# Optimization experiments

Measured on AMD Instinct MI355X. Metric: run time of the kernel, lower is better.

Reference implementation:

```python
import jax, jax.numpy as jnp
import numpy as np

# Config constants (MLAConfig)
B, S = 1, 2048                 # batch, context_len (prefill: seq == context_len)
H = 16                         # num_heads
DN, DR, DV = 128, 64, 128      # qk_nope_head_dim, qk_rope_head_dim, v_head_dim
QL, C = 1536, 512              # q_lora_rank, kv_lora_rank
BLK = 128                      # fp8 dequant block size
MAX_CACHE = 4096
SOFTMAX_SCALE = 1.0 / np.sqrt(DN + DR)  # 1/sqrt(192)
NEG_INF = -10000.0


def gen_rope(n_total, head_size):
    # theta_j = 10000^{-2j/d}; idx_theta[i, 0, :] = [i*theta, i*theta] (repeated halves)
    theta = 1.0 / (10000.0 ** (jnp.arange(0, head_size, 2, dtype=jnp.float32) / head_size))
    idx = jnp.outer(jnp.arange(n_total, dtype=jnp.float32), theta)  # (N, d/2)
    return jnp.tile(idx[:, None, :], (1, 1, 2))                     # (N, 1, d)


def fp8_dequant(x, s, block=BLK):
    # Block-wise dequant: x (M,N) * per-(block x block) scale s (M/b, N/b).
    M, N = x.shape
    m, n = M // block, N // block  # shapes chosen divisible by block -> no padding
    return (x.reshape(m, block, n, block) * s[:, None, :, None]).reshape(M, N)


def apply_rope(x, cos, sin):
    # x: (B*S, heads, d). Interleaved RoPE: de-interleave pairs into halves,
    # then x*cos + rotate_half(x)*sin with cos/sin (B*S, 1, d).
    bs, h, d = x.shape
    x = x.reshape(bs, h, d // 2, 2).transpose(0, 1, 3, 2).reshape(bs, h, d)
    rot = jnp.concatenate([-x[..., d // 2:], x[..., :d // 2]], axis=-1)
    return x * cos + rot * sin


def setup_inputs() -> dict:
    key = jax.random.key(0)
    ks = jax.random.split(key, 9)
    WUQ = jax.random.normal(ks[0], (H * (DN + DR), QL), dtype=jnp.float32)
    WUKV = jax.random.normal(ks[1], (H * (DN + DV), C), dtype=jnp.float32)
    # positive, small block scales so attention logits stay well-conditioned
    WUQ_scale = 0.05 * jax.random.uniform(ks[2], (H * (DN + DR) // BLK, QL // BLK), dtype=jnp.float32)
    WUKV_scale = 0.05 * jax.random.uniform(ks[3], (H * (DN + DV) // BLK, C // BLK), dtype=jnp.float32)
    Q = jax.random.normal(ks[4], (B, S, QL), dtype=jnp.float32)
    KV = jax.random.normal(ks[5], (B, S, C), dtype=jnp.float32)
    PE = jax.random.normal(ks[6], (B, S, DR), dtype=jnp.float32)
    kv_cache = jax.random.normal(ks[7], (B, MAX_CACHE, C), dtype=jnp.float32)
    pe_cache = jax.random.normal(ks[8], (B, MAX_CACHE, DR), dtype=jnp.float32)
    idx_theta = gen_rope(B * S, DR)
    mask = jnp.triu(jnp.full((S, S), NEG_INF, dtype=jnp.float32), k=1)
    return {"WUQ": WUQ, "WUQ_scale": WUQ_scale, "WUKV": WUKV, "WUKV_scale": WUKV_scale,
            "Q": Q, "KV": KV, "PE": PE, "kv_cache": kv_cache, "pe_cache": pe_cache,
            "idx_theta": idx_theta, "mask": mask}


def reference(WUQ, WUQ_scale, WUKV, WUKV_scale, Q, KV, PE, kv_cache, pe_cache, idx_theta, mask):
    bsz, seqlen, _ = Q.shape
    # fp8 block-wise dequant of the low-rank up-projection weights
    WUQd = fp8_dequant(WUQ, WUQ_scale)
    WUKVd = fp8_dequant(WUKV, WUKV_scale)
    # Q up-projection from q_lora latent: (B*S, QL) @ (QL, H*(DN+DR))
    q = (Q.reshape(-1, QL) @ WUQd.T).reshape(bsz, seqlen, H, DN + DR)
    q_nope, q_pe = q[..., :DN], q[..., DN:]
    cos, sin = jnp.cos(idx_theta), jnp.sin(idx_theta)  # (B*S, 1, DR)
    q_pe = apply_rope(q_pe.reshape(bsz * seqlen, H, DR), cos, sin).reshape(bsz, seqlen, H, DR)
    k_pe = apply_rope(PE.reshape(bsz * seqlen, 1, DR), cos, sin).reshape(bsz, seqlen, DR)
    # absorbed low-rank K matrix: q_nope projected into the kv latent space
    W3 = WUKVd.reshape(H, DN + DV, C)
    q_lat = jnp.einsum('bshd,hdc->bshc', q_nope, W3[:, :DN])
    # continuous-cache prefill: write fresh latents into the cache, attend over them
    kv = kv_cache.at[:, :seqlen].set(KV)[:, :seqlen]   # (B, S, C)
    pe = pe_cache.at[:, :seqlen].set(k_pe)[:, :seqlen]  # (B, S, DR)
    scores = (jnp.einsum('bshc,btc->bsht', q_lat, kv)
              + jnp.einsum('bshr,btr->bsht', q_pe, pe)) * SOFTMAX_SCALE
    scores = scores + mask[None, :, None, :]
    attn = jax.nn.softmax(scores, axis=-1)
    x = jnp.einsum('bsht,btc->bshc', attn, kv)
    out = jnp.einsum('bshc,hdc->bshd', x, W3[:, DN:])  # V up-projection (absorbed)
    return out  # (B, S, H, DV)
```

## Files before the change

### kernel.cpp

```cpp
#include <hip/hip_runtime.h>

typedef __bf16 bf16_t;
typedef __attribute__((ext_vector_type(4))) __bf16 bf16x4;
typedef __attribute__((ext_vector_type(8))) __bf16 bf16x8;
typedef __attribute__((ext_vector_type(4))) float f32x4;

#define SOFTMAX_SCALE 0.07216878364870322f
#define NEG_MASK (-10000.0f)

__device__ __forceinline__ void async16(const bf16_t* g, bf16_t* l) {
  __builtin_amdgcn_global_load_lds(
      (const __attribute__((address_space(1))) unsigned int*)g,
      (__attribute__((address_space(3))) unsigned int*)l, 16, 0, 0);
}

__global__ void k_prep(const float* __restrict__ WUQ, const float* __restrict__ WUQs,
                       bf16_t* __restrict__ WUQd,
                       const float* __restrict__ WUKV, const float* __restrict__ WUKVs,
                       bf16_t* __restrict__ WUKVd, bf16_t* __restrict__ Wv1t,
                       const float* __restrict__ Q, bf16_t* __restrict__ Qb,
                       const float* __restrict__ KV, bf16_t* __restrict__ K4,
                       bf16_t* __restrict__ V4,
                       const float* __restrict__ PE, const float* __restrict__ idxt) {
  __shared__ bf16_t Lt[64][72];
  const int b = blockIdx.x;
  const int tid = threadIdx.x;

  if (b < 4608) {
    int i = (b * 256 + tid) * 4;
    int r = i / 1536, c = i % 1536;
    float s = WUQs[(r >> 7) * 12 + (c >> 7)];
    float4 w = *(const float4*)(WUQ + i);
    WUQd[i + 0] = (bf16_t)(w.x * s);
    WUQd[i + 1] = (bf16_t)(w.y * s);
    WUQd[i + 2] = (bf16_t)(w.z * s);
    WUQd[i + 3] = (bf16_t)(w.w * s);
  } else if (b < 5632) {
    int i4 = ((b - 4608) * 256 + tid) * 4;
    int h = i4 >> 16, within = i4 & 65535;
    int row = 128 + (within >> 9), col = within & 511;
    int R = h * 256 + row;
    float s = WUKVs[(R >> 7) * 4 + (col >> 7)];
    const float* src = WUKV + (size_t)R * 512 + col;
    float4 w = *(const float4*)src;
    bf16_t* dst = WUKVd + (size_t)R * 512 + col;
    dst[0] = (bf16_t)(w.x * s);
    dst[1] = (bf16_t)(w.y * s);
    dst[2] = (bf16_t)(w.z * s);
    dst[3] = (bf16_t)(w.w * s);
  } else if (b < 8704) {
    int i = ((b - 5632) * 256 + tid) * 4;
    float4 v = *(const float4*)(Q + i);
    Qb[i + 0] = (bf16_t)(v.x * SOFTMAX_SCALE);
    Qb[i + 1] = (bf16_t)(v.y * SOFTMAX_SCALE);
    Qb[i + 2] = (bf16_t)(v.z * SOFTMAX_SCALE);
    Qb[i + 3] = (bf16_t)(v.w * SOFTMAX_SCALE);
  } else if (b < 8832) {
    int i = (b - 8704) * 256 + tid;
    int c2 = i & 15, t = i >> 4;
    int tt = t >> 6, k = t & 63;
    const float* src = KV + (size_t)t * 512 + c2 * 32;
    bf16_t* dst = K4 + (size_t)tt * 36864 + c2 * 2048 + k * 8;
#pragma unroll
    for (int sub = 0; sub < 4; ++sub) {
      float4 u = *(const float4*)(src + sub * 8);
      float4 v = *(const float4*)(src + sub * 8 + 4);
      bf16x8 o;
      o[0] = (bf16_t)u.x; o[1] = (bf16_t)u.y; o[2] = (bf16_t)u.z; o[3] = (bf16_t)u.w;
      o[4] = (bf16_t)v.x; o[5] = (bf16_t)v.y; o[6] = (bf16_t)v.z; o[7] = (bf16_t)v.w;
      *(bf16x8*)(dst + sub * 512) = o;
    }
  } else if (b < 9344) {
    int i = (b - 8832) * 256 + tid;
    int c = i & 511, a = i >> 9;
    int t0 = a * 8, tt = t0 >> 6;
    int key0 = t0 & 63, kk2 = key0 >> 5, sub = (key0 >> 3) & 3;
    bf16x8 o;
#pragma unroll
    for (int j = 0; j < 8; ++j)
      o[j] = (bf16_t)KV[(size_t)(t0 + j) * 512 + c];
    *(bf16x8*)(V4 + (size_t)tt * 32768 + kk2 * 16384 + sub * 4096 + c * 8) = o;
  } else if (b < 9600) {
    int i = (b - 9344) * 256 + tid;
    int t = i >> 5, j = i & 31;
    float a = idxt[t * 64 + j];
    float c1 = cosf(a), s1 = sinf(a);
    float e = PE[t * 64 + 2 * j], o = PE[t * 64 + 2 * j + 1];
    int tt = t >> 6, k = t & 63;
    bf16_t* base = K4 + (size_t)tt * 36864 + (j >> 3) * 512 + k * 8 + (j & 7);
    base[16 * 2048] = (bf16_t)(e * c1 - o * s1);
    base[17 * 2048] = (bf16_t)(o * c1 + e * s1);
  } else {
    int bb = b - 9600;
    int h = bb >> 4;
    int d0 = ((bb >> 3) & 1) * 64;
    int c0 = (bb & 7) * 64;
    float s = WUKVs[8 * h + (c0 >> 7)];
#pragma unroll
    for (int j = 0; j < 2; ++j) {
      int ch = tid * 2 + j, r = ch >> 3, c8 = ch & 7;
      const float* src = WUKV + (size_t)(h * 256 + d0 + r) * 512 + c0 + c8 * 8;
      float4 u = *(const float4*)src;
      float4 v = *(const float4*)(src + 4);
      bf16x8 o;
      o[0] = (bf16_t)(u.x * s); o[1] = (bf16_t)(u.y * s);
      o[2] = (bf16_t)(u.z * s); o[3] = (bf16_t)(u.w * s);
      o[4] = (bf16_t)(v.x * s); o[5] = (bf16_t)(v.y * s);
      o[6] = (bf16_t)(v.z * s); o[7] = (bf16_t)(v.w * s);
      *(bf16x8*)&Lt[r][c8 * 8] = o;
    }
    __syncthreads();
#pragma unroll
    for (int j = 0; j < 2; ++j) {
      int ch = tid * 2 + j, cc = ch >> 3, dd8 = ch & 7;
      bf16x8 o;
#pragma unroll
      for (int e = 0; e < 8; ++e) o[e] = Lt[dd8 * 8 + e][cc];
      *(bf16x8*)(Wv1t + (size_t)h * 65536 + (c0 + cc) * 128 + d0 + dd8 * 8) = o;
    }
  }
}

__global__ void k_q_rope(const bf16_t* __restrict__ q, const float* __restrict__ idxt,
                         bf16_t* __restrict__ qfull) {
  int i = blockIdx.x * 256 + threadIdx.x;
  int j = i & 31, h = (i >> 5) & 15, t = i >> 9;
  float a = idxt[t * 64 + j];
  float c1 = cosf(a), s1 = sinf(a);
  const bf16_t* src = q + t * 3072 + h * 192 + 128;
  float e = (float)src[2 * j], o = (float)src[2 * j + 1];
  bf16_t* dst = qfull + (size_t)h * 2048 * 576 + t * 576 + 512;
  dst[j]      = (bf16_t)(e * c1 - o * s1);
  dst[32 + j] = (bf16_t)(o * c1 + e * s1);
}

template <int OUT_F32>
__global__ __launch_bounds__(256) void k_gemm3(
    const bf16_t* __restrict__ A, int lda, long saz,
    const bf16_t* __restrict__ B, int ldb, long sbz,
    void* __restrict__ Cv, int ldc, long scz, int K) {
  __shared__ __attribute__((aligned(16))) bf16_t At[2][8192];
  __shared__ __attribute__((aligned(16))) bf16_t Bt[2][8192];
  const int tid = threadIdx.x;
  const int lane = tid & 63;
  const int wv = tid >> 6;
  const int fr = lane & 15, fq = lane >> 4;
  const int wm = (wv & 1) * 64, wn = (wv >> 1) * 64;
  const int m0 = blockIdx.x * 128, n0 = blockIdx.y * 128;
  const bf16_t* Ab = A + (long)blockIdx.z * saz;
  const bf16_t* Bb = B + (long)blockIdx.z * sbz;

#define STAGE3(bufp, ks)                                                    \
  do {                                                                      \
    _Pragma("unroll") for (int i_ = 0; i_ < 4; ++i_) {                      \
      int ch_ = tid + i_ * 256;                                             \
      int ar_ = ch_ >> 3;                                                   \
      int c8_ = (ch_ & 7) ^ (ar_ & 7);                                      \
      async16(Ab + (size_t)(m0 + ar_) * lda + (ks) * 64 + c8_ * 8,          \
              At[bufp] + ch_ * 8);                                          \
      async16(Bb + (size_t)(n0 + ar_) * ldb + (ks) * 64 + c8_ * 8,          \
              Bt[bufp] + ch_ * 8);                                          \
    }                                                                       \
  } while (0)

  f32x4 acc[4][4] = {};
  const int nks = K >> 6;
  STAGE3(0, 0);
  for (int ks = 0; ks < nks; ++ks) {
    int buf = ks & 1;
    __syncthreads();
    if (ks + 1 < nks) STAGE3(buf ^ 1, ks + 1);
#pragma unroll
    for (int kkl = 0; kkl < 2; ++kkl) {
      bf16x8 af[4], bfr[4];
#pragma unroll
      for (int m = 0; m < 4; ++m) {
        int row = wm + m * 16 + fr;
        af[m] = *(const bf16x8*)(At[buf] + (row * 8 + (((kkl * 4 + fq) ^ (row & 7)))) * 8);
      }
#pragma unroll
      for (int n = 0; n < 4; ++n) {
        int row = wn + n * 16 + fr;
        bfr[n] = *(const bf16x8*)(Bt[buf] + (row * 8 + (((kkl * 4 + fq) ^ (row & 7)))) * 8);
      }
#pragma unroll
      for (int m = 0; m < 4; ++m)
#pragma unroll
        for (int n = 0; n < 4; ++n)
          acc[m][n] = __builtin_amdgcn_mfma_f32_16x16x32_bf16(af[m], bfr[n], acc[m][n], 0, 0, 0);
    }
  }
#undef STAGE3
#pragma unroll
  for (int m = 0; m < 4; ++m) {
    int row = m0 + wm + m * 16 + fq * 4;
#pragma unroll
    for (int n = 0; n < 4; ++n) {
      int col = n0 + wn + n * 16 + fr;
#pragma unroll
      for (int i = 0; i < 4; ++i) {
        if (OUT_F32)
          ((float*)Cv)[(long)blockIdx.z * scz + (size_t)(row + i) * ldc + col] = acc[m][n][i];
        else
          ((bf16_t*)Cv)[(long)blockIdx.z * scz + (size_t)(row + i) * ldc + col] = (bf16_t)acc[m][n][i];
      }
    }
  }
}

__global__ __attribute__((amdgpu_flat_work_group_size(512, 512),
                          amdgpu_waves_per_eu(2, 2)))
void k_attn(const bf16_t* __restrict__ qfull,
            const bf16_t* __restrict__ K4,
            const bf16_t* __restrict__ V4,
            bf16_t* __restrict__ X) {
  __shared__ __attribute__((aligned(16))) bf16_t Kt[18 * 2048];
  __shared__ __attribute__((aligned(16))) bf16_t Vt[2 * 16384];
  __shared__ __attribute__((aligned(16))) bf16_t P[64 * 64];
  __shared__ __attribute__((aligned(16))) bf16_t Qpe[8 * 512];
  __shared__ float lred[4][64];

  const int tid = threadIdx.x;
  const int lane = tid & 63;
  const int w = tid >> 6;
  const int fr = lane & 15, fq = lane >> 4;
  const int h = blockIdx.x & 15;
  const int qt = 31 - (blockIdx.x >> 4);
  const int nt = qt + 1;
  const int rg = w >> 2;
  const int kq = w & 3;

  const bf16_t* qh = qfull + (size_t)h * 2048 * 576;
  bf16_t* Xh = X + (size_t)h * 2048 * 512;

  {
    int row = tid >> 3, sub = tid & 7;
    bf16x8 v = *(const bf16x8*)(qh + (size_t)(qt * 64 + row) * 576 + 512 + sub * 8);
    *(bf16x8*)(Qpe + sub * 512 + row * 8) = v;
  }

  bf16x8 qa[2][16];
  {
    const bf16_t* qb = qh + (size_t)(qt * 64 + rg * 32) * 576;
#pragma unroll
    for (int mf = 0; mf < 2; ++mf)
#pragma unroll
      for (int kk = 0; kk < 16; ++kk)
        qa[mf][kk] = *(const bf16x8*)(qb + (mf * 16 + fr) * 576 + kk * 32 + fq * 8);
  }

#pragma unroll
  for (int i = 0; i < 9; ++i) {
    int ck = w + 8 * i;
    async16(K4 + ck * 512 + lane * 8, Kt + ck * 512 + lane * 8);
  }

  f32x4 acc[2][8] = {};
  float lreg[2] = {0.f, 0.f};

  for (int t = 0; t < nt; ++t) {
    __syncthreads();

    {
      const bf16_t* vsrc = V4 + (size_t)t * 32768;
#pragma unroll
      for (int i = 0; i < 8; ++i) {
        int cv = w + 8 * i;
        async16(vsrc + cv * 512 + lane * 8, Vt + cv * 512 + lane * 8);
      }
    }

    f32x4 sA[2] = {}, sB[2] = {};
    __builtin_amdgcn_s_setprio(1);
#pragma unroll
    for (int kk = 0; kk < 16; kk += 2) {
      bf16x8 kf0 = *(const bf16x8*)(Kt + kk * 2048 + fq * 512 + (kq * 16 + fr) * 8);
      bf16x8 kf1 = *(const bf16x8*)(Kt + (kk + 1) * 2048 + fq * 512 + (kq * 16 + fr) * 8);
      sA[0] = __builtin_amdgcn_mfma_f32_16x16x32_bf16(kf0, qa[0][kk], sA[0], 0, 0, 0);
      sA[1] = __builtin_amdgcn_mfma_f32_16x16x32_bf16(kf0, qa[1][kk], sA[1], 0, 0, 0);
      sB[0] = __builtin_amdgcn_mfma_f32_16x16x32_bf16(kf1, qa[0][kk + 1], sB[0], 0, 0, 0);
      sB[1] = __builtin_amdgcn_mfma_f32_16x16x32_bf16(kf1, qa[1][kk + 1], sB[1], 0, 0, 0);
    }
    {
      bf16x8 kf0 = *(const bf16x8*)(Kt + 16 * 2048 + fq * 512 + (kq * 16 + fr) * 8);
      bf16x8 kf1 = *(const bf16x8*)(Kt + 17 * 2048 + fq * 512 + (kq * 16 + fr) * 8);
      bf16x8 q00 = *(const bf16x8*)(Qpe + fq * 512 + (rg * 32 + fr) * 8);
      bf16x8 q01 = *(const bf16x8*)(Qpe + fq * 512 + (rg * 32 + 16 + fr) * 8);
      bf16x8 q10 = *(const bf16x8*)(Qpe + (4 + fq) * 512 + (rg * 32 + fr) * 8);
      bf16x8 q11 = *(const bf16x8*)(Qpe + (4 + fq) * 512 + (rg * 32 + 16 + fr) * 8);
      sA[0] = __builtin_amdgcn_mfma_f32_16x16x32_bf16(kf0, q00, sA[0], 0, 0, 0);
      sA[1] = __builtin_amdgcn_mfma_f32_16x16x32_bf16(kf0, q01, sA[1], 0, 0, 0);
      sB[0] = __builtin_amdgcn_mfma_f32_16x16x32_bf16(kf1, q10, sB[0], 0, 0, 0);
      sB[1] = __builtin_amdgcn_mfma_f32_16x16x32_bf16(kf1, q11, sB[1], 0, 0, 0);
    }
    __builtin_amdgcn_s_setprio(0);
    f32x4 s[2];
#pragma unroll
    for (int mf = 0; mf < 2; ++mf)
#pragma unroll
      for (int i = 0; i < 4; ++i) s[mf][i] = sA[mf][i] + sB[mf][i];

    bool diag = (t == qt);
#pragma unroll
    for (int mf = 0; mf < 2; ++mf) {
      int qrow = rg * 32 + mf * 16 + fr;
      if (diag) {
#pragma unroll
        for (int i = 0; i < 4; ++i) {
          int kcol = kq * 16 + fq * 4 + i;
          if (kcol > qrow) s[mf][i] += NEG_MASK;
        }
      }
      float p0 = __expf(s[mf][0]);
      float p1 = __expf(s[mf][1]);
      float p2 = __expf(s[mf][2]);
      float p3 = __expf(s[mf][3]);
      bf16x4 pk;
      pk[0] = (bf16_t)p0; pk[1] = (bf16_t)p1; pk[2] = (bf16_t)p2; pk[3] = (bf16_t)p3;
      int chunk = (kq * 2 + (fq >> 1)) ^ (qrow & 7);
      *(bf16x4*)(P + qrow * 64 + chunk * 8 + (fq & 1) * 4) = pk;
      lreg[mf] += (p0 + p1) + (p2 + p3);
    }
    __syncthreads();

    if (t + 1 < nt) {
      const bf16_t* ksrc = K4 + (size_t)(t + 1) * 36864;
#pragma unroll
      for (int i = 0; i < 9; ++i) {
        int ck = w + 8 * i;
        async16(ksrc + ck * 512 + lane * 8, Kt + ck * 512 + lane * 8);
      }
    }

    __builtin_amdgcn_s_setprio(1);
#pragma unroll
    for (int kk2 = 0; kk2 < 2; ++kk2) {
      bf16x8 pa[2];
#pragma unroll
      for (int mf = 0; mf < 2; ++mf) {
        int qrow = rg * 32 + mf * 16 + fr;
        pa[mf] = *(const bf16x8*)(P + qrow * 64 + (((kk2 * 4 + fq) ^ (qrow & 7)) * 8));
      }
#pragma unroll
      for (int nf = 0; nf < 8; ++nf) {
        bf16x8 vb = *(const bf16x8*)(Vt + kk2 * 16384 + fq * 4096 + (kq * 128 + nf * 16 + fr) * 8);
        acc[0][nf] = __builtin_amdgcn_mfma_f32_16x16x32_bf16(pa[0], vb, acc[0][nf], 0, 0, 0);
        acc[1][nf] = __builtin_amdgcn_mfma_f32_16x16x32_bf16(pa[1], vb, acc[1][nf], 0, 0, 0);
      }
    }
    __builtin_amdgcn_s_setprio(0);
  }

#pragma unroll
  for (int mf = 0; mf < 2; ++mf) {
    float lw = lreg[mf];
    lw += __shfl_xor(lw, 16);
    lw += __shfl_xor(lw, 32);
    if (fq == 0) lred[kq][rg * 32 + mf * 16 + fr] = lw;
  }
  __syncthreads();

  {
    bf16_t* XT = Kt;
#pragma unroll
    for (int mf = 0; mf < 2; ++mf)
#pragma unroll
      for (int i = 0; i < 4; ++i) {
        int row = rg * 32 + mf * 16 + fq * 4 + i;
        float invl = 1.0f / ((lred[0][row] + lred[1][row]) + (lred[2][row] + lred[3][row]));
#pragma unroll
        for (int nf = 0; nf < 8; ++nf)
          XT[row * 512 + kq * 128 + nf * 16 + fr] = (bf16_t)(acc[mf][nf][i] * invl);
      }
  }
  __syncthreads();
#pragma unroll
  for (int it = 0; it < 8; ++it) {
    int id = tid + it * 512;
    int row = id >> 6, j = id & 63;
    *(bf16x8*)(Xh + (size_t)(qt * 64 + row) * 512 + j * 8) = *(const bf16x8*)(Kt + row * 512 + j * 8);
  }
}


extern "C" void kernel_launch(void* const* d_in, const int* in_sizes, int n_in,
                              void* d_out, int out_size, void* d_ws, size_t ws_size,
                              hipStream_t stream) {
  (void)in_sizes; (void)n_in; (void)out_size; (void)ws_size;
  const float* WUQ   = (const float*)d_in[0];
  const float* WUQs  = (const float*)d_in[1];
  const float* WUKV  = (const float*)d_in[2];
  const float* WUKVs = (const float*)d_in[3];
  const float* Q     = (const float*)d_in[4];
  const float* KV    = (const float*)d_in[5];
  const float* PE    = (const float*)d_in[6];
  const float* idxt  = (const float*)d_in[9];
  float* out = (float*)d_out;

  char* ws = (char*)d_ws;
  size_t off = 0;
  auto alloc = [&](size_t n) -> char* {
    char* p = ws + off;
    off += (n + 255) & ~(size_t)255;
    return p;
  };
  bf16_t* WUQd  = (bf16_t*)alloc((size_t)3072 * 1536 * 2);
  bf16_t* Qb    = (bf16_t*)alloc((size_t)2048 * 1536 * 2);
  bf16_t* WUKVd = (bf16_t*)alloc((size_t)4096 * 512 * 2);
  bf16_t* Wv1t  = (bf16_t*)alloc((size_t)16 * 512 * 128 * 2);
  bf16_t* qbuf  = (bf16_t*)alloc((size_t)2048 * 3072 * 2);
  bf16_t* K4    = (bf16_t*)alloc((size_t)32 * 36864 * 2);
  bf16_t* V4    = (bf16_t*)alloc((size_t)32 * 32768 * 2);
  bf16_t* qfull = (bf16_t*)alloc((size_t)16 * 2048 * 576 * 2);
  bf16_t* Xb    = (bf16_t*)alloc((size_t)16 * 2048 * 512 * 2);

  k_prep<<<9856, 256, 0, stream>>>(WUQ, WUQs, WUQd, WUKV, WUKVs, WUKVd, Wv1t,
                                   Q, Qb, KV, K4, V4, PE, idxt);
  k_gemm3<0><<<dim3(16, 24, 1), 256, 0, stream>>>(Qb, 1536, 0, WUQd, 1536, 0,
                                                  qbuf, 3072, 0, 1536);
  k_q_rope<<<4096, 256, 0, stream>>>(qbuf, idxt, qfull);
  k_gemm3<0><<<dim3(16, 4, 16), 256, 0, stream>>>(qbuf, 3072, 192, Wv1t, 128, (long)512 * 128,
                                                  qfull, 576, (long)2048 * 576, 128);
  k_attn<<<dim3(512), dim3(512), 0, stream>>>(qfull, K4, V4, Xb);
  k_gemm3<1><<<dim3(16, 1, 16), 256, 0, stream>>>(Xb, 512, (long)2048 * 512,
                                                  WUKVd + 128 * 512, 512, (long)256 * 512,
                                                  out, 2048, 128, 512);
}
```

Baseline: 194.6 us.

## Software-pipeline attention loop: overlap next tile's QK with current softmax and PV

Restructures the causal attention tile loop into prologue/steady-state/epilogue so that QK^T MFMAs for tile t are interleaved with the exp/P-store of tile t-1 and followed by PV of tile t-1. The diagonal masking moves to the epilogue since only the last tile is diagonal. This aims to hide the softmax VALU latency behind matrix work. In exchange it keeps two score sets live, which raises register pressure, and it drops the split sA/sB accumulators that gave two independent MFMA chains. When nt==1 it issues a redundant K reload.

```diff
diff --git a/kernel.cpp b/kernel.cpp
--- a/kernel.cpp
+++ b/kernel.cpp
@@ -257,64 +257,127 @@
 
   f32x4 acc[2][8] = {};
   float lreg[2] = {0.f, 0.f};
-
-  for (int t = 0; t < nt; ++t) {
-    __syncthreads();
-
-    {
-      const bf16_t* vsrc = V4 + (size_t)t * 32768;
-#pragma unroll
-      for (int i = 0; i < 8; ++i) {
-        int cv = w + 8 * i;
-        async16(vsrc + cv * 512 + lane * 8, Vt + cv * 512 + lane * 8);
-      }
-    }
-
-    f32x4 sA[2] = {}, sB[2] = {};
+  f32x4 sO[2];
+
+#define QK_CHUNKS(K0, K1)                                                      \
+  do {                                                                         \
+    _Pragma("unroll") for (int kk = (K0); kk < (K1); ++kk) {                   \
+      bf16x8 kf = *(const bf16x8*)(Kt + kk * 2048 + fq * 512 + (kq * 16 + fr) * 8); \
+      sN[0] = __builtin_amdgcn_mfma_f32_16x16x32_bf16(kf, qa[0][kk], sN[0], 0, 0, 0); \
+      sN[1] = __builtin_amdgcn_mfma_f32_16x16x32_bf16(kf, qa[1][kk], sN[1], 0, 0, 0); \
+    }                                                                          \
+  } while (0)
+
+#define QK_PE()                                                                \
+  do {                                                                         \
+    _Pragma("unroll") for (int kk = 16; kk < 18; ++kk) {                       \
+      bf16x8 kf = *(const bf16x8*)(Kt + kk * 2048 + fq * 512 + (kq * 16 + fr) * 8); \
+      bf16x8 q0 = *(const bf16x8*)(Qpe + ((kk - 16) * 4 + fq) * 512 + (rg * 32 + fr) * 8); \
+      bf16x8 q1 = *(const bf16x8*)(Qpe + ((kk - 16) * 4 + fq) * 512 + (rg * 32 + 16 + fr) * 8); \
+      sN[0] = __builtin_amdgcn_mfma_f32_16x16x32_bf16(kf, q0, sN[0], 0, 0, 0);  \
+      sN[1] = __builtin_amdgcn_mfma_f32_16x16x32_bf16(kf, q1, sN[1], 0, 0, 0);  \
+    }                                                                          \
+  } while (0)
+
+#define EXP_P()                                                                \
+  do {                                                                         \
+    _Pragma("unroll") for (int mf = 0; mf < 2; ++mf) {                         \
+      int qrow = rg * 32 + mf * 16 + fr;                                       \
+      float p0 = __expf(sO[mf][0]);                                            \
+      float p1 = __expf(sO[mf][1]);                                            \
+      float p2 = __expf(sO[mf][2]);                                            \
+      float p3 = __expf(sO[mf][3]);                                            \
+      bf16x4 pk;                                                               \
+      pk[0] = (bf16_t)p0; pk[1] = (bf16_t)p1; pk[2] = (bf16_t)p2; pk[3] = (bf16_t)p3; \
+      int chunk = (kq * 2 + (fq >> 1)) ^ (qrow & 7);                           \
+      *(bf16x4*)(P + qrow * 64 + chunk * 8 + (fq & 1) * 4) = pk;               \
+      lreg[mf] += (p0 + p1) + (p2 + p3);                                       \
+    }                                                                          \
+  } while (0)
+
+#define PV()                                                                   \
+  do {                                                                         \
+    __builtin_amdgcn_s_setprio(1);                                             \
+    _Pragma("unroll") for (int kk2 = 0; kk2 < 2; ++kk2) {                      \
+      bf16x8 pa[2];                                                            \
+      _Pragma("unroll") for (int mf = 0; mf < 2; ++mf) {                       \
+        int qrow = rg * 32 + mf * 16 + fr;                                     \
+        pa[mf] = *(const bf16x8*)(P + qrow * 64 + (((kk2 * 4 + fq) ^ (qrow & 7)) * 8)); \
+      }                                                                        \
+      _Pragma("unroll") for (int nf = 0; nf < 8; ++nf) {                       \
+        bf16x8 vb = *(const bf16x8*)(Vt + kk2 * 16384 + fq * 4096 + (kq * 128 + nf * 16 + fr) * 8); \
+        acc[0][nf] = __builtin_amdgcn_mfma_f32_16x16x32_bf16(pa[0], vb, acc[0][nf], 0, 0, 0); \
+        acc[1][nf] = __builtin_amdgcn_mfma_f32_16x16x32_bf16(pa[1], vb, acc[1][nf], 0, 0, 0); \
+      }                                                                        \
+    }                                                                          \
+    __builtin_amdgcn_s_setprio(0);                                             \
+  } while (0)
+
+#define ISSUE_V(tv)                                                            \
+  do {                                                                         \
+    const bf16_t* vsrc_ = V4 + (size_t)(tv) * 32768;                           \
+    _Pragma("unroll") for (int i_ = 0; i_ < 8; ++i_) {                         \
+      int cv_ = w + 8 * i_;                                                    \
+      async16(vsrc_ + cv_ * 512 + lane * 8, Vt + cv_ * 512 + lane * 8);        \
+    }                                                                          \
+  } while (0)
+
+#define ISSUE_K(tk)                                                            \
+  do {                                                                         \
+    const bf16_t* ksrc_ = K4 + (size_t)(tk) * 36864;                           \
+    _Pragma("unroll") for (int i_ = 0; i_ < 9; ++i_) {                         \
+      int ck_ = w + 8 * i_;                                                    \
+      async16(ksrc_ + ck_ * 512 + lane * 8, Kt + ck_ * 512 + lane * 8);        \
+    }                                                                          \
+  } while (0)
+
+  {
+    __syncthreads();
+    f32x4 sN[2] = {};
     __builtin_amdgcn_s_setprio(1);
-#pragma unroll
-    for (int kk = 0; kk < 16; kk += 2) {
-      bf16x8 kf0 = *(const bf16x8*)(Kt + kk * 2048 + fq * 512 + (kq * 16 + fr) * 8);
-      bf16x8 kf1 = *(const bf16x8*)(Kt + (kk + 1) * 2048 + fq * 512 + (kq * 16 + fr) * 8);
-      sA[0] = __builtin_amdgcn_mfma_f32_16x16x32_bf16(kf0, qa[0][kk], sA[0], 0, 0, 0);
-      sA[1] = __builtin_amdgcn_mfma_f32_16x16x32_bf16(kf0, qa[1][kk], sA[1], 0, 0, 0);
-      sB[0] = __builtin_amdgcn_mfma_f32_16x16x32_bf16(kf1, qa[0][kk + 1], sB[0], 0, 0, 0);
-      sB[1] = __builtin_amdgcn_mfma_f32_16x16x32_bf16(kf1, qa[1][kk + 1], sB[1], 0, 0, 0);
-    }
-    {
-      bf16x8 kf0 = *(const bf16x8*)(Kt + 16 * 2048 + fq * 512 + (kq * 16 + fr) * 8);
-      bf16x8 kf1 = *(const bf16x8*)(Kt + 17 * 2048 + fq * 512 + (kq * 16 + fr) * 8);
-      bf16x8 q00 = *(const bf16x8*)(Qpe + fq * 512 + (rg * 32 + fr) * 8);
-      bf16x8 q01 = *(const bf16x8*)(Qpe + fq * 512 + (rg * 32 + 16 + fr) * 8);
-      bf16x8 q10 = *(const bf16x8*)(Qpe + (4 + fq) * 512 + (rg * 32 + fr) * 8);
-      bf16x8 q11 = *(const bf16x8*)(Qpe + (4 + fq) * 512 + (rg * 32 + 16 + fr) * 8);
-      sA[0] = __builtin_amdgcn_mfma_f32_16x16x32_bf16(kf0, q00, sA[0], 0, 0, 0);
-      sA[1] = __builtin_amdgcn_mfma_f32_16x16x32_bf16(kf0, q01, sA[1], 0, 0, 0);
-      sB[0] = __builtin_amdgcn_mfma_f32_16x16x32_bf16(kf1, q10, sB[0], 0, 0, 0);
-      sB[1] = __builtin_amdgcn_mfma_f32_16x16x32_bf16(kf1, q11, sB[1], 0, 0, 0);
-    }
+    QK_CHUNKS(0, 16);
+    QK_PE();
     __builtin_amdgcn_s_setprio(0);
-    f32x4 s[2];
-#pragma unroll
-    for (int mf = 0; mf < 2; ++mf)
-#pragma unroll
-      for (int i = 0; i < 4; ++i) s[mf][i] = sA[mf][i] + sB[mf][i];
-
-    bool diag = (t == qt);
+    sO[0] = sN[0]; sO[1] = sN[1];
+    __syncthreads();
+    int tn = (1 < nt) ? 1 : 0;
+    ISSUE_K(tn);
+  }
+
+  for (int t = 1; t < nt; ++t) {
+    __syncthreads();
+    ISSUE_V(t - 1);
+    f32x4 sN[2] = {};
+    __builtin_amdgcn_s_setprio(1);
+    QK_CHUNKS(0, 10);
+    __builtin_amdgcn_s_setprio(0);
+    EXP_P();
+    __builtin_amdgcn_s_setprio(1);
+    QK_CHUNKS(10, 16);
+    QK_PE();
+    __builtin_amdgcn_s_setprio(0);
+    __syncthreads();
+    int tn = (t + 1 < nt) ? t + 1 : nt - 1;
+    ISSUE_K(tn);
+    PV();
+    sO[0] = sN[0]; sO[1] = sN[1];
+  }
+
+  {
+    __syncthreads();
+    ISSUE_V(nt - 1);
 #pragma unroll
     for (int mf = 0; mf < 2; ++mf) {
       int qrow = rg * 32 + mf * 16 + fr;
-      if (diag) {
-#pragma unroll
-        for (int i = 0; i < 4; ++i) {
-          int kcol = kq * 16 + fq * 4 + i;
-          if (kcol > qrow) s[mf][i] += NEG_MASK;
-        }
+#pragma unroll
+      for (int i = 0; i < 4; ++i) {
+        int kcol = kq * 16 + fq * 4 + i;
+        if (kcol > qrow) sO[mf][i] += NEG_MASK;
       }
-      float p0 = __expf(s[mf][0]);
-      float p1 = __expf(s[mf][1]);
-      float p2 = __expf(s[mf][2]);
-      float p3 = __expf(s[mf][3]);
+      float p0 = __expf(sO[mf][0]);
+      float p1 = __expf(sO[mf][1]);
+      float p2 = __expf(sO[mf][2]);
+      float p3 = __expf(sO[mf][3]);
       bf16x4 pk;
       pk[0] = (bf16_t)p0; pk[1] = (bf16_t)p1; pk[2] = (bf16_t)p2; pk[3] = (bf16_t)p3;
       int chunk = (kq * 2 + (fq >> 1)) ^ (qrow & 7);
@@ -322,34 +385,15 @@
       lreg[mf] += (p0 + p1) + (p2 + p3);
     }
     __syncthreads();
-
-    if (t + 1 < nt) {
-      const bf16_t* ksrc = K4 + (size_t)(t + 1) * 36864;
-#pragma unroll
-      for (int i = 0; i < 9; ++i) {
-        int ck = w + 8 * i;
-        async16(ksrc + ck * 512 + lane * 8, Kt + ck * 512 + lane * 8);
-      }
-    }
-
-    __builtin_amdgcn_s_setprio(1);
-#pragma unroll
-    for (int kk2 = 0; kk2 < 2; ++kk2) {
-      bf16x8 pa[2];
-#pragma unroll
-      for (int mf = 0; mf < 2; ++mf) {
-        int qrow = rg * 32 + mf * 16 + fr;
-        pa[mf] = *(const bf16x8*)(P + qrow * 64 + (((kk2 * 4 + fq) ^ (qrow & 7)) * 8));
-      }
-#pragma unroll
-      for (int nf = 0; nf < 8; ++nf) {
-        bf16x8 vb = *(const bf16x8*)(Vt + kk2 * 16384 + fq * 4096 + (kq * 128 + nf * 16 + fr) * 8);
-        acc[0][nf] = __builtin_amdgcn_mfma_f32_16x16x32_bf16(pa[0], vb, acc[0][nf], 0, 0, 0);
-        acc[1][nf] = __builtin_amdgcn_mfma_f32_16x16x32_bf16(pa[1], vb, acc[1][nf], 0, 0, 0);
-      }
-    }
-    __builtin_amdgcn_s_setprio(0);
-  }
+    PV();
+  }
+
+#undef QK_CHUNKS
+#undef QK_PE
+#undef EXP_P
+#undef PV
+#undef ISSUE_V
+#undef ISSUE_K
 
 #pragma unroll
   for (int mf = 0; mf < 2; ++mf) {
```

New measurement: 242.6 us. +24.6%, slower.
